# Kernel optimization log

Measured on AMD Instinct MI355X. Metric: run time of the kernel, lower is better.

Reference implementation:

```python
import jax, jax.numpy as jnp
import numpy as np

H = 16        # query heads
KVH = 4       # kv heads
DK = 64       # head dim
D = H * DK    # d_model = 1024
R = 16        # lora rank
SCALING = 16.0 / 16.0 * 1.0   # alpha/rank*scale
ALIBI_ALPHA = 1.0
NEG = jnp.finfo(jnp.float32).min


def _lora_linear(x, W, A, Bm):
    # nn.Linear(bias=False) + LoRA: x@W + (x@A@B)*scaling
    return x @ W + (x @ A @ Bm) * SCALING


def setup_inputs() -> dict:
    key = jax.random.key(0)
    ks = jax.random.split(key, 16)
    B, S = 2, 2048
    f = jnp.float32
    return {
        "query": jax.random.normal(ks[0], (B, S, D), f),
        "key": jax.random.normal(ks[1], (B, S, D), f),
        "value": jax.random.normal(ks[2], (B, S, D), f),
        "Wq": jax.random.normal(ks[3], (D, D), f) * 0.02,
        "Wk": jax.random.normal(ks[4], (D, KVH * DK), f) * 0.02,
        "Wv": jax.random.normal(ks[5], (D, KVH * DK), f) * 0.02,
        "Wo": jax.random.normal(ks[6], (D, D), f) * 0.02,
        "Aq": jax.random.normal(ks[7], (D, R), f) * 0.02,
        "Bq": jax.random.normal(ks[8], (R, D), f) * 0.02,
        "Ak": jax.random.normal(ks[9], (D, R), f) * 0.02,
        "Bk": jax.random.normal(ks[10], (R, KVH * DK), f) * 0.02,
        "Av": jax.random.normal(ks[11], (D, R), f) * 0.02,
        "Bv": jax.random.normal(ks[12], (R, KVH * DK), f) * 0.02,
        "Ao": jax.random.normal(ks[13], (D, R), f) * 0.02,
        "Bo": jax.random.normal(ks[14], (R, D), f) * 0.02,
    }


def _attention(query, key, value, Wq, Wk, Wv, Wo, Aq, Bq, Ak, Bk, Av, Bv, Ao, Bo):
    B, Sq, _ = query.shape
    Sk = key.shape[1]
    groups = H // KVH

    Q = _lora_linear(query, Wq, Aq, Bq).reshape(B, Sq, H, DK).transpose(0, 2, 1, 3)     # (B,H,Sq,DK)
    K = _lora_linear(key, Wk, Ak, Bk).reshape(B, Sk, KVH, DK).transpose(0, 2, 1, 3)      # (B,KVH,Sk,DK)
    V = _lora_linear(value, Wv, Av, Bv).reshape(B, Sk, KVH, DK).transpose(0, 2, 1, 3)

    # GQA: repeat_interleave kv heads to match query heads
    K = jnp.repeat(K, groups, axis=1)   # (B,H,Sk,DK)
    V = jnp.repeat(V, groups, axis=1)

    scale = 1.0 / np.sqrt(DK).astype(np.float32)
    scores = (jnp.einsum('bhqd,bhkd->bhqk', Q, K) * scale).astype(jnp.float32)

    # ALiBi: bias[h,q,k] = slope_h * (k - q), slopes = 2^(-alpha*(i+start)), i=1..H
    slopes = (2.0 ** (-ALIBI_ALPHA * jnp.arange(1, H + 1, dtype=jnp.float32)))
    q_idx = jnp.arange(Sq, dtype=jnp.float32)[:, None]
    k_idx = jnp.arange(Sk, dtype=jnp.float32)[None, :]
    scores = scores + slopes[None, :, None, None] * (k_idx - q_idx)[None, None, :, :]

    # causal mask (keep lower triangle)
    causal = jnp.tril(jnp.ones((Sq, Sk), dtype=bool))
    scores = jnp.where(causal[None, None], scores, NEG)

    attn = jax.nn.softmax(scores, axis=-1).astype(Q.dtype)   # dropout is identity in eval
    x = jnp.einsum('bhqk,bhkd->bhqd', attn, V)
    x = x.transpose(0, 2, 1, 3).reshape(B, Sq, D)
    return _lora_linear(x, Wo, Ao, Bo)


def reference(query, key, value, Wq, Wk, Wv, Wo, Aq, Bq, Ak, Bk, Av, Bv, Ao, Bo):
    return _attention(query, key, value, Wq, Wk, Wv, Wo, Aq, Bq, Ak, Bk, Av, Bv, Ao, Bo)
```

## Files before the change

kernel.cpp:

```cpp
#include <hip/hip_runtime.h>
#include <hip/hip_bf16.h>


typedef __attribute__((ext_vector_type(8))) short short8;
typedef __attribute__((ext_vector_type(4))) float f32x4;
typedef __attribute__((ext_vector_type(16))) float f32x16;
typedef __attribute__((ext_vector_type(2))) unsigned int uint2v;
typedef __attribute__((ext_vector_type(4))) unsigned short ushort4v;

#define DEV static __device__ __forceinline__

DEV unsigned short f32_to_bf16(float f) {
  unsigned int u = __float_as_uint(f);
  u += 0x7FFFu + ((u >> 16) & 1u);
  return (unsigned short)(u >> 16);
}

DEV unsigned int cvt_pk_bf16(float lo, float hi) {
  unsigned int r;
  asm("v_cvt_pk_bf16_f32 %0, %1, %2" : "=v"(r) : "v"(lo), "v"(hi));
  return r;
}

DEV float fexp2(float x) { return __builtin_amdgcn_exp2f(x); }

DEV short8 cvt8(f32x4 a, f32x4 b) {
  short8 r;
  r[0] = (short)f32_to_bf16(a[0]); r[1] = (short)f32_to_bf16(a[1]);
  r[2] = (short)f32_to_bf16(a[2]); r[3] = (short)f32_to_bf16(a[3]);
  r[4] = (short)f32_to_bf16(b[0]); r[5] = (short)f32_to_bf16(b[1]);
  r[6] = (short)f32_to_bf16(b[2]); r[7] = (short)f32_to_bf16(b[3]);
  return r;
}

DEV void gld16(const unsigned short* g, unsigned short* l) {
  __builtin_amdgcn_global_load_lds(
      (const __attribute__((address_space(1))) void*)g,
      (__attribute__((address_space(3))) void*)l,
      16, 0, 0);
}

DEV int xcd_chunk(int bid, int nblk) {
  const int chunk = nblk >> 3;
  return (bid & 7) * chunk + (bid >> 3);
}

__global__ __launch_bounds__(256) void weff_all_kernel(
    const float* __restrict__ Wq, const float* __restrict__ Aq, const float* __restrict__ Bq, unsigned short* __restrict__ WqT,
    const float* __restrict__ Wk, const float* __restrict__ Ak, const float* __restrict__ Bk, unsigned short* __restrict__ WkT,
    const float* __restrict__ Wv, const float* __restrict__ Av, const float* __restrict__ Bv, unsigned short* __restrict__ WvT,
    const float* __restrict__ Wo, const float* __restrict__ Ao, const float* __restrict__ Bo, unsigned short* __restrict__ WoT) {
  __shared__ float tile[16][17];
  const int bx = blockIdx.x;
  const float *W, *A, *Bm; unsigned short* WT; int N, nb;
  if (bx < 64)       { W = Wq; A = Aq; Bm = Bq; WT = WqT; N = 1024; nb = bx; }
  else if (bx < 80)  { W = Wk; A = Ak; Bm = Bk; WT = WkT; N = 256;  nb = bx - 64; }
  else if (bx < 96)  { W = Wv; A = Av; Bm = Bv; WT = WvT; N = 256;  nb = bx - 80; }
  else               { W = Wo; A = Ao; Bm = Bo; WT = WoT; N = 1024; nb = bx - 96; }
  const int tx = threadIdx.x, ty = threadIdx.y;
  const int n0 = nb * 16, k0 = blockIdx.y * 16;
  const int n = n0 + tx, k = k0 + ty;
  float acc = W[(size_t)k * N + n];
#pragma unroll
  for (int r = 0; r < 16; ++r) acc += A[k * 16 + r] * Bm[(size_t)r * N + n];
  tile[ty][tx] = acc;
  __syncthreads();
  WT[(size_t)(n0 + ty) * 1024 + (k0 + tx)] = f32_to_bf16(tile[tx][ty]);
}

__global__ __launch_bounds__(256) void cast3_kernel(const float* __restrict__ q,
                                                    const float* __restrict__ k,
                                                    const float* __restrict__ v,
                                                    unsigned short* __restrict__ oq,
                                                    unsigned short* __restrict__ ok,
                                                    unsigned short* __restrict__ ov) {
  const int seg = blockIdx.x >> 11;
  const size_t off = ((size_t)(blockIdx.x & 2047) * 256 + threadIdx.x) * 8;
  const float* src = (seg == 0) ? q : (seg == 1) ? k : v;
  unsigned short* dst = (seg == 0) ? oq : (seg == 1) ? ok : ov;
  f32x4 a = *(const f32x4*)(src + off);
  f32x4 b = *(const f32x4*)(src + off + 4);
  *(short8*)(dst + off) = cvt8(a, b);
}

template <int OUTMODE>
DEV void gemm97_core(const unsigned short* __restrict__ X,
                     const unsigned short* __restrict__ WT,
                     void* __restrict__ Cv, int N, int m0b, int n0b,
                     unsigned short* lds) {
  constexpr int K = 1024, BK = 64, NT = K / BK;
  constexpr int ASZ = 64 * 64;
  constexpr int BUFE = ASZ + 128 * 64;
  const int tid = threadIdx.x;
  const int w = tid >> 6, l = tid & 63;
  const int lr = l & 15, lg = l >> 4;
  const int wm = w >> 1, wn = w & 1;
  const int srow = l >> 3, schunk = l & 7;

  const unsigned short* Xrow0 = X + (size_t)m0b * K;
  const unsigned short* Wrow0 = WT + (size_t)n0b * K;

  f32x4 acc[2][4];
#pragma unroll
  for (int mm = 0; mm < 2; ++mm)
#pragma unroll
    for (int nn = 0; nn < 4; ++nn) acc[mm][nn] = f32x4{0.f, 0.f, 0.f, 0.f};

#define STAGE(T, BUF)                                                        \
  {                                                                          \
    unsigned short* Ab_ = lds + (BUF) * BUFE;                                \
    unsigned short* Bb_ = Ab_ + ASZ;                                         \
    const int k0_ = (T) * BK;                                                \
    _Pragma("unroll")                                                        \
    for (int ii = 0; ii < 2; ++ii) {                                         \
      const int inst_ = 2 * w + ii;                                          \
      const int row_ = inst_ * 8 + srow;                                     \
      const int cs_ = (schunk ^ (row_ & 7)) * 8;                             \
      gld16(Xrow0 + (size_t)row_ * K + k0_ + cs_, Ab_ + inst_ * 512);        \
    }                                                                        \
    _Pragma("unroll")                                                        \
    for (int ii = 0; ii < 4; ++ii) {                                         \
      const int inst_ = 4 * w + ii;                                          \
      const int row_ = inst_ * 8 + srow;                                     \
      const int cs_ = (schunk ^ (row_ & 7)) * 8;                             \
      gld16(Wrow0 + (size_t)row_ * K + k0_ + cs_, Bb_ + inst_ * 512);        \
    }                                                                        \
  }

  STAGE(0, 0)
  __syncthreads();
  int cur = 0;

  for (int t = 0; t < NT; ++t) {
    if (t + 1 < NT) STAGE(t + 1, cur ^ 1)

    const unsigned short* Ab = lds + cur * BUFE;
    const unsigned short* Bb = Ab + ASZ;
    short8 af[2][2], bfg[4][2];
#pragma unroll
    for (int kk = 0; kk < 2; ++kk) {
#pragma unroll
      for (int mm = 0; mm < 2; ++mm) {
        const int row = wm * 32 + mm * 16 + lr;
        const int cc = ((kk * 4 + lg) ^ (row & 7)) * 8;
        af[mm][kk] = *(const short8*)(Ab + row * 64 + cc);
      }
#pragma unroll
      for (int nn = 0; nn < 4; ++nn) {
        const int row = wn * 64 + nn * 16 + lr;
        const int cc = ((kk * 4 + lg) ^ (row & 7)) * 8;
        bfg[nn][kk] = *(const short8*)(Bb + row * 64 + cc);
      }
    }

#pragma unroll
    for (int kk = 0; kk < 2; ++kk)
#pragma unroll
      for (int mm = 0; mm < 2; ++mm)
#pragma unroll
        for (int nn = 0; nn < 4; ++nn)
          acc[mm][nn] = __builtin_amdgcn_mfma_f32_16x16x32_bf16(af[mm][kk], bfg[nn][kk], acc[mm][nn], 0, 0, 0);

    __syncthreads();
    cur ^= 1;
  }
#undef STAGE

#pragma unroll
  for (int mm = 0; mm < 2; ++mm)
#pragma unroll
    for (int nn = 0; nn < 4; ++nn)
#pragma unroll
      for (int i = 0; i < 4; ++i) {
        const int row = m0b + wm * 32 + mm * 16 + lg * 4 + i;
        const int col = n0b + wn * 64 + nn * 16 + lr;
        const float v = acc[mm][nn][i];
        if (OUTMODE == 0) {
          ((unsigned short*)Cv)[(size_t)row * N + col] = f32_to_bf16(v);
        } else if (OUTMODE == 1) {
          ((float*)Cv)[(size_t)row * N + col] = v;
        } else if (OUTMODE == 2) {
          ((unsigned short*)Cv)[((size_t)((row >> 11) * 4 + (col >> 6)) * 64 + (col & 63)) * 2048 + (row & 2047)] = f32_to_bf16(v);
        } else {
          ((unsigned short*)Cv)[((size_t)((row >> 11) * 4 + (col >> 6)) * 2048 + (row & 2047)) * 64 + (col & 63)] = f32_to_bf16(v);
        }
      }
}

__global__ __launch_bounds__(256, 3) void qkv_kernel(
    const unsigned short* __restrict__ Xq, const unsigned short* __restrict__ Xk, const unsigned short* __restrict__ Xv,
    const unsigned short* __restrict__ WqT, const unsigned short* __restrict__ WkT, const unsigned short* __restrict__ WvT,
    unsigned short* __restrict__ Qw, unsigned short* __restrict__ Khm, unsigned short* __restrict__ Vtw) {
  __shared__ __align__(16) unsigned short lds[2 * (64 * 64 + 128 * 64)];
  const int bx = blockIdx.x;
  if (bx < 512) {
    const int v = xcd_chunk(bx, 512);
    gemm97_core<0>(Xq, WqT, Qw, 1024, (v >> 3) * 64, (v & 7) * 128, lds);
  } else if (bx < 640) {
    const int v = xcd_chunk(bx - 512, 128);
    gemm97_core<3>(Xk, WkT, Khm, 256, (v >> 1) * 64, (v & 1) * 128, lds);
  } else {
    const int v = xcd_chunk(bx - 640, 128);
    gemm97_core<2>(Xv, WvT, Vtw, 256, (v >> 1) * 64, (v & 1) * 128, lds);
  }
}

__global__ __launch_bounds__(256, 3) void ogemm_kernel(const unsigned short* __restrict__ Xw,
                                                       const unsigned short* __restrict__ WoT,
                                                       float* __restrict__ out) {
  __shared__ __align__(16) unsigned short lds[2 * (64 * 64 + 128 * 64)];
  const int v = xcd_chunk(blockIdx.x, 512);
  gemm97_core<1>(Xw, WoT, out, 1024, (v >> 3) * 64, (v & 7) * 128, lds);
}

__global__ __launch_bounds__(512, 4) void attn8_kernel(const unsigned short* __restrict__ Q,
                                                       const unsigned short* __restrict__ Kh,
                                                       const unsigned short* __restrict__ Vt,
                                                       unsigned short* __restrict__ Xo) {
  __shared__ __align__(16) unsigned short sbuf[2][2][2][4096];

  const int tid = threadIdx.x;
  const int l = tid & 63, w = tid >> 6;
  const int cq = l & 31, hi = l >> 5;
  const int qc = w & 3, par = w >> 2;

  const int bid = blockIdx.x;
  const int half = bid >> 8, p = bid & 255;
  const int h = p & 15, b = (p >> 4) & 1, j = p >> 5;
  const int qt = half ? j : 15 - j;

  const int kv = h >> 2;
  const int qw0 = qt * 128 + qc * 32;
  const int q = qw0 + cq;
  const float LOG2E = 1.44269504f;
  const float slope2 = fexp2(-(float)(h + 1)) * LOG2E;
  const float qscale = 0.125f * LOG2E;

  const unsigned short* qp = Q + ((size_t)(b * 2048 + q)) * 1024 + h * 64 + hi * 8;
  short8 qf[4];
#pragma unroll
  for (int c = 0; c < 4; ++c) qf[c] = *(const short8*)(qp + c * 16);

  const int nit = qt + 1;
  const int nktw = (qw0 + 31) / 64 + 1;

  const unsigned short* Kg = Kh + (size_t)(b * 4 + kv) * 2048 * 64;
  const unsigned short* Vg = Vt + (size_t)(b * 4 + kv) * 64 * 2048;
  const int srow = tid >> 3;
  const int scol = (tid & 7) ^ (srow & 7);
  const unsigned short* ksrc = Kg + srow * 64 + scol * 8;
  const unsigned short* vsrc = Vg + (size_t)srow * 2048 + scol * 8;
  const size_t woff = (size_t)w * 512;

#define STAGE(IT, B_)                                                       \
  {                                                                         \
    const int kb_ = (IT) * 128;                                             \
    gld16(ksrc + (size_t)kb_ * 64,        &sbuf[B_][0][0][woff]);           \
    gld16(ksrc + (size_t)(kb_ + 64) * 64, &sbuf[B_][0][1][woff]);           \
    gld16(vsrc + kb_,                     &sbuf[B_][1][0][woff]);           \
    gld16(vsrc + kb_ + 64,                &sbuf[B_][1][1][woff]);           \
  }

  STAGE(0, 0)
  __syncthreads();
  int cur = 0;

  f32x16 oA, oB;
#pragma unroll
  for (int r = 0; r < 16; ++r) { oA[r] = 0.f; oB[r] = 0.f; }
  float mrun = -3e38f, lrun = 0.f;

  const float fhi = 4.0f * (float)hi;
  const int sx = cq & 7;
  const int rA = cq, rB = cq + 32;

  for (int it = 0; it < nit; ++it) {
    if (it + 1 < nit) STAGE(it + 1, cur ^ 1)

    const int kt = 2 * it + par;
    if (kt < nktw) {
      const int k0 = kt * 64;
      const unsigned short* Kl = &sbuf[cur][0][par][0];
      const unsigned short* Vl = &sbuf[cur][1][par][0];

      f32x16 sA, sB;
#pragma unroll
      for (int r = 0; r < 16; ++r) { sA[r] = 0.f; sB[r] = 0.f; }
      __builtin_amdgcn_s_setprio(1);
#pragma unroll
      for (int c = 0; c < 4; ++c) {
        short8 ka = *(const short8*)(Kl + rA * 64 + (((c * 2 + hi) ^ sx) * 8));
        short8 kb = *(const short8*)(Kl + rB * 64 + (((c * 2 + hi) ^ sx) * 8));
        sA = __builtin_amdgcn_mfma_f32_32x32x16_bf16(ka, qf[c], sA, 0, 0, 0);
        sB = __builtin_amdgcn_mfma_f32_32x32x16_bf16(kb, qf[c], sB, 0, 0, 0);
      }
      __builtin_amdgcn_s_setprio(0);

      const float fhb   = fmaf(slope2, fhi, slope2 * (float)(k0 - q));
      const float fhb32 = fmaf(slope2, fhi, slope2 * (float)(k0 + 32 - q));
      const bool masked = (kt == nktw - 1);
      const int ikq4 = k0 - q + 4 * hi;
      float svA[16], svB[16];
#pragma unroll
      for (int r = 0; r < 16; ++r) {
        const int koffc = (r & 3) + 8 * (r >> 2);
        const float kf = (float)koffc;
        float va = fmaf(sA[r], qscale, fmaf(slope2, kf, fhb));
        float vb = fmaf(sB[r], qscale, fmaf(slope2, kf, fhb32));
        if (masked) {
          if (ikq4 + koffc > 0) va = -3e38f;
          if (ikq4 + koffc + 32 > 0) vb = -3e38f;
        }
        svA[r] = va; svB[r] = vb;
      }

      float m0_ = fmaxf(svA[0], svB[0]), m1_ = fmaxf(svA[1], svB[1]);
      float m2_ = fmaxf(svA[2], svB[2]), m3_ = fmaxf(svA[3], svB[3]);
#pragma unroll
      for (int r = 4; r < 16; r += 4) {
        m0_ = fmaxf(m0_, fmaxf(svA[r], svB[r]));
        m1_ = fmaxf(m1_, fmaxf(svA[r + 1], svB[r + 1]));
        m2_ = fmaxf(m2_, fmaxf(svA[r + 2], svB[r + 2]));
        m3_ = fmaxf(m3_, fmaxf(svA[r + 3], svB[r + 3]));
      }
      float mx = fmaxf(fmaxf(m0_, m1_), fmaxf(m2_, m3_));
      mx = fmaxf(mx, __shfl_xor(mx, 32));

      if (!__all(mx <= mrun + 8.0f)) {
        const float mnew = fmaxf(mrun, mx);
        const float fsc = fexp2(mrun - mnew);
        lrun *= fsc;
        mrun = mnew;
#pragma unroll
        for (int r = 0; r < 16; ++r) { oA[r] *= fsc; oB[r] *= fsc; }
      }

      float pA[16], pB[16];
      float l0_ = 0.f, l1_ = 0.f, l2_ = 0.f, l3_ = 0.f;
#pragma unroll
      for (int r = 0; r < 16; r += 4) {
        pA[r] = fexp2(svA[r] - mrun);         pB[r] = fexp2(svB[r] - mrun);
        pA[r + 1] = fexp2(svA[r + 1] - mrun); pB[r + 1] = fexp2(svB[r + 1] - mrun);
        pA[r + 2] = fexp2(svA[r + 2] - mrun); pB[r + 2] = fexp2(svB[r + 2] - mrun);
        pA[r + 3] = fexp2(svA[r + 3] - mrun); pB[r + 3] = fexp2(svB[r + 3] - mrun);
        l0_ += pA[r] + pB[r];
        l1_ += pA[r + 1] + pB[r + 1];
        l2_ += pA[r + 2] + pB[r + 2];
        l3_ += pA[r + 3] + pB[r + 3];
      }
      float ls = (l0_ + l1_) + (l2_ + l3_);
      ls += __shfl_xor(ls, 32);
      lrun += ls;

#define PV_HALF(PARR, KHALF)                                                          \
      {                                                                               \
        _Pragma("unroll")                                                             \
        for (int g = 0; g < 2; ++g) {                                                 \
          unsigned int a0 = cvt_pk_bf16(PARR[g * 8 + 0], PARR[g * 8 + 1]);            \
          unsigned int b0 = cvt_pk_bf16(PARR[g * 8 + 4], PARR[g * 8 + 5]);            \
          unsigned int a1 = cvt_pk_bf16(PARR[g * 8 + 2], PARR[g * 8 + 3]);            \
          unsigned int b1 = cvt_pk_bf16(PARR[g * 8 + 6], PARR[g * 8 + 7]);            \
          uint2v r0 = __builtin_amdgcn_permlane32_swap(a0, b0, false, false);         \
          uint2v r1 = __builtin_amdgcn_permlane32_swap(a1, b1, false, false);         \
          union { unsigned int u[4]; short8 s; } pb_;                                 \
          pb_.u[0] = r0[0]; pb_.u[1] = r1[0]; pb_.u[2] = r0[1]; pb_.u[3] = r1[1];     \
          const int c16 = ((KHALF) * 4 + g * 2 + hi) ^ sx;                            \
          short8 v0 = *(const short8*)(Vl + rA * 64 + c16 * 8);                       \
          short8 v1 = *(const short8*)(Vl + rB * 64 + c16 * 8);                       \
          __builtin_amdgcn_s_setprio(1);                                              \
          oA = __builtin_amdgcn_mfma_f32_32x32x16_bf16(v0, pb_.s, oA, 0, 0, 0);       \
          oB = __builtin_amdgcn_mfma_f32_32x32x16_bf16(v1, pb_.s, oB, 0, 0, 0);       \
          __builtin_amdgcn_s_setprio(0);                                              \
        }                                                                             \
      }
      PV_HALF(pA, 0)
      PV_HALF(pB, 1)
#undef PV_HALF
    }

    __syncthreads();
    cur ^= 1;
  }
#undef STAGE

  float* obuf = (float*)&sbuf[0][0][0][0];
  float* mlb  = obuf + 128 * 68;
  const int orow = (qc * 32 + cq) * 68;

  if (par == 1) {
#pragma unroll
    for (int g = 0; g < 4; ++g) {
      f32x4 t0 = {oA[g * 4 + 0], oA[g * 4 + 1], oA[g * 4 + 2], oA[g * 4 + 3]};
      f32x4 t1 = {oB[g * 4 + 0], oB[g * 4 + 1], oB[g * 4 + 2], oB[g * 4 + 3]};
      *(f32x4*)&obuf[orow + g * 8 + 4 * hi] = t0;
      *(f32x4*)&obuf[orow + 32 + g * 8 + 4 * hi] = t1;
    }
    if (hi == 0) {
      mlb[(qc * 32 + cq) * 2] = mrun;
      mlb[(qc * 32 + cq) * 2 + 1] = lrun;
    }
  }
  __syncthreads();
  if (par == 0) {
    const float m1v = mlb[(qc * 32 + cq) * 2];
    const float l1v = mlb[(qc * 32 + cq) * 2 + 1];
    const float ms = fmaxf(mrun, m1v);
    const float s0 = fexp2(mrun - ms), s1 = fexp2(m1v - ms);
    const float rinv = __builtin_amdgcn_rcpf(fmaf(lrun, s0, l1v * s1));
    unsigned short* op = Xo + ((size_t)(b * 2048 + q)) * 1024 + h * 64;
#pragma unroll
    for (int g = 0; g < 4; ++g) {
      const int d0 = g * 8 + 4 * hi;
      f32x4 u0 = *(const f32x4*)&obuf[orow + d0];
      f32x4 u1 = *(const f32x4*)&obuf[orow + 32 + d0];
      ushort4v t0, t1;
#pragma unroll
      for (int i = 0; i < 4; ++i) {
        t0[i] = f32_to_bf16(fmaf(oA[g * 4 + i], s0, u0[i] * s1) * rinv);
        t1[i] = f32_to_bf16(fmaf(oB[g * 4 + i], s0, u1[i] * s1) * rinv);
      }
      *(ushort4v*)(op + d0) = t0;
      *(ushort4v*)(op + 32 + d0) = t1;
    }
  }
}

extern "C" void kernel_launch(void* const* d_in, const int* in_sizes, int n_in,
                              void* d_out, int out_size, void* d_ws, size_t ws_size,
                              hipStream_t stream) {
  const float* query = (const float*)d_in[0];
  const float* key   = (const float*)d_in[1];
  const float* value = (const float*)d_in[2];
  const float* Wq = (const float*)d_in[3];
  const float* Wk = (const float*)d_in[4];
  const float* Wv = (const float*)d_in[5];
  const float* Wo = (const float*)d_in[6];
  const float* Aq = (const float*)d_in[7];
  const float* Bq = (const float*)d_in[8];
  const float* Ak = (const float*)d_in[9];
  const float* Bk = (const float*)d_in[10];
  const float* Av = (const float*)d_in[11];
  const float* Bv = (const float*)d_in[12];
  const float* Ao = (const float*)d_in[13];
  const float* Bo = (const float*)d_in[14];

  unsigned short* ws  = (unsigned short*)d_ws;
  unsigned short* WqT = ws;
  unsigned short* WkT = WqT + 1024 * 1024;
  unsigned short* WvT = WkT + 256 * 1024;
  unsigned short* WoT = WvT + 256 * 1024;
  unsigned short* Qw  = WoT + 1024 * 1024;
  unsigned short* Khm = Qw + 4096 * 1024;
  unsigned short* Vtw = Khm + 4096 * 256;
  unsigned short* Xw  = Vtw + 4096 * 256;
  unsigned short* Xcq = Xw + 4096 * 1024;
  unsigned short* Xck = Xcq + 4096 * 1024;

  weff_all_kernel<<<dim3(160, 64), dim3(16, 16), 0, stream>>>(
      Wq, Aq, Bq, WqT, Wk, Ak, Bk, WkT, Wv, Av, Bv, WvT, Wo, Ao, Bo, WoT);

  cast3_kernel<<<6144, 256, 0, stream>>>(query, key, value, Xcq, Xck, Xw);

  qkv_kernel<<<768, 256, 0, stream>>>(Xcq, Xck, Xw, WqT, WkT, WvT, Qw, Khm, Vtw);

  attn8_kernel<<<512, 512, 0, stream>>>(Qw, Khm, Vtw, Xw);

  ogemm_kernel<<<512, 256, 0, stream>>>(Xw, WoT, (float*)d_out);
}
```

Baseline: 101.2 us.

## Split attention KV across four waves per block and fuse prep kernels

The attention kernel now gives each block 64 query rows instead of 128, and the key dimension is split four ways across wave pairs, with a 4-way softmax merge through LDS at the end. The grid doubles to 1024 blocks, scheduled longest-first. K/V tiles are loaded 256 keys at a time into a single buffer, with no double-buffered prefetch. Separately, the weight-merge and input-cast kernels are fused into one launch to remove a kernel launch. The risk is that dropping the prefetch exposes load latency, and the merge costs more LDS traffic.

```diff
diff --git a/kernel.cpp b/kernel.cpp
--- a/kernel.cpp
+++ b/kernel.cpp
@@ -45,42 +45,41 @@
   return (bid & 7) * chunk + (bid >> 3);
 }
 
-__global__ __launch_bounds__(256) void weff_all_kernel(
+__global__ __launch_bounds__(256) void prep_kernel(
     const float* __restrict__ Wq, const float* __restrict__ Aq, const float* __restrict__ Bq, unsigned short* __restrict__ WqT,
     const float* __restrict__ Wk, const float* __restrict__ Ak, const float* __restrict__ Bk, unsigned short* __restrict__ WkT,
     const float* __restrict__ Wv, const float* __restrict__ Av, const float* __restrict__ Bv, unsigned short* __restrict__ WvT,
-    const float* __restrict__ Wo, const float* __restrict__ Ao, const float* __restrict__ Bo, unsigned short* __restrict__ WoT) {
+    const float* __restrict__ Wo, const float* __restrict__ Ao, const float* __restrict__ Bo, unsigned short* __restrict__ WoT,
+    const float* __restrict__ q, const float* __restrict__ k, const float* __restrict__ v,
+    unsigned short* __restrict__ oq, unsigned short* __restrict__ ok, unsigned short* __restrict__ ov) {
+  const int bx = blockIdx.x;
+  if (bx < 6144) {
+    const int seg = bx >> 11;
+    const size_t off = ((size_t)(bx & 2047) * 256 + threadIdx.x) * 8;
+    const float* src = (seg == 0) ? q : (seg == 1) ? k : v;
+    unsigned short* dst = (seg == 0) ? oq : (seg == 1) ? ok : ov;
+    f32x4 a = *(const f32x4*)(src + off);
+    f32x4 b = *(const f32x4*)(src + off + 4);
+    *(short8*)(dst + off) = cvt8(a, b);
+    return;
+  }
   __shared__ float tile[16][17];
-  const int bx = blockIdx.x;
+  const int wb = bx - 6144;
+  const int nbx = wb % 160, kby = wb / 160;
   const float *W, *A, *Bm; unsigned short* WT; int N, nb;
-  if (bx < 64)       { W = Wq; A = Aq; Bm = Bq; WT = WqT; N = 1024; nb = bx; }
-  else if (bx < 80)  { W = Wk; A = Ak; Bm = Bk; WT = WkT; N = 256;  nb = bx - 64; }
-  else if (bx < 96)  { W = Wv; A = Av; Bm = Bv; WT = WvT; N = 256;  nb = bx - 80; }
-  else               { W = Wo; A = Ao; Bm = Bo; WT = WoT; N = 1024; nb = bx - 96; }
-  const int tx = threadIdx.x, ty = threadIdx.y;
-  const int n0 = nb * 16, k0 = blockIdx.y * 16;
-  const int n = n0 + tx, k = k0 + ty;
-  float acc = W[(size_t)k * N + n];
-#pragma unroll
-  for (int r = 0; r < 16; ++r) acc += A[k * 16 + r] * Bm[(size_t)r * N + n];
+  if (nbx < 64)       { W = Wq; A = Aq; Bm = Bq; WT = WqT; N = 1024; nb = nbx; }
+  else if (nbx < 80)  { W = Wk; A = Ak; Bm = Bk; WT = WkT; N = 256;  nb = nbx - 64; }
+  else if (nbx < 96)  { W = Wv; A = Av; Bm = Bv; WT = WvT; N = 256;  nb = nbx - 80; }
+  else                { W = Wo; A = Ao; Bm = Bo; WT = WoT; N = 1024; nb = nbx - 96; }
+  const int tx = threadIdx.x & 15, ty = threadIdx.x >> 4;
+  const int n0 = nb * 16, k0 = kby * 16;
+  const int n = n0 + tx, kk = k0 + ty;
+  float acc = W[(size_t)kk * N + n];
+#pragma unroll
+  for (int r = 0; r < 16; ++r) acc += A[kk * 16 + r] * Bm[(size_t)r * N + n];
   tile[ty][tx] = acc;
   __syncthreads();
   WT[(size_t)(n0 + ty) * 1024 + (k0 + tx)] = f32_to_bf16(tile[tx][ty]);
-}
-
-__global__ __launch_bounds__(256) void cast3_kernel(const float* __restrict__ q,
-                                                    const float* __restrict__ k,
-                                                    const float* __restrict__ v,
-                                                    unsigned short* __restrict__ oq,
-                                                    unsigned short* __restrict__ ok,
-                                                    unsigned short* __restrict__ ov) {
-  const int seg = blockIdx.x >> 11;
-  const size_t off = ((size_t)(blockIdx.x & 2047) * 256 + threadIdx.x) * 8;
-  const float* src = (seg == 0) ? q : (seg == 1) ? k : v;
-  unsigned short* dst = (seg == 0) ? oq : (seg == 1) ? ok : ov;
-  f32x4 a = *(const f32x4*)(src + off);
-  f32x4 b = *(const f32x4*)(src + off + 4);
-  *(short8*)(dst + off) = cvt8(a, b);
 }
 
 template <int OUTMODE>
@@ -213,24 +212,25 @@
   gemm97_core<1>(Xw, WoT, out, 1024, (v >> 3) * 64, (v & 7) * 128, lds);
 }
 
-__global__ __launch_bounds__(512, 4) void attn8_kernel(const unsigned short* __restrict__ Q,
+__global__ __launch_bounds__(512, 4) void attn9_kernel(const unsigned short* __restrict__ Q,
                                                        const unsigned short* __restrict__ Kh,
                                                        const unsigned short* __restrict__ Vt,
                                                        unsigned short* __restrict__ Xo) {
-  __shared__ __align__(16) unsigned short sbuf[2][2][2][4096];
+  __shared__ __align__(16) unsigned short sbuf[2][4][4096];
 
   const int tid = threadIdx.x;
   const int l = tid & 63, w = tid >> 6;
   const int cq = l & 31, hi = l >> 5;
-  const int qc = w & 3, par = w >> 2;
+  const int cq2 = w & 1, ks = w >> 1;
 
   const int bid = blockIdx.x;
-  const int half = bid >> 8, p = bid & 255;
-  const int h = p & 15, b = (p >> 4) & 1, j = p >> 5;
-  const int qt = half ? j : 15 - j;
+  const int s = 31 - (bid >> 5);
+  const int rem = bid & 31;
+  const int h = rem & 15, b = rem >> 4;
 
   const int kv = h >> 2;
-  const int qw0 = qt * 128 + qc * 32;
+  const int c_abs = 2 * s + cq2;
+  const int qw0 = c_abs * 32;
   const int q = qw0 + cq;
   const float LOG2E = 1.44269504f;
   const float slope2 = fexp2(-(float)(h + 1)) * LOG2E;
@@ -241,8 +241,8 @@
 #pragma unroll
   for (int c = 0; c < 4; ++c) qf[c] = *(const short8*)(qp + c * 16);
 
-  const int nit = qt + 1;
-  const int nktw = (qw0 + 31) / 64 + 1;
+  const int T = (c_abs >> 1) + 1;
+  const int NI = (s + 4) >> 2;
 
   const unsigned short* Kg = Kh + (size_t)(b * 4 + kv) * 2048 * 64;
   const unsigned short* Vg = Vt + (size_t)(b * 4 + kv) * 64 * 2048;
@@ -252,19 +252,6 @@
   const unsigned short* vsrc = Vg + (size_t)srow * 2048 + scol * 8;
   const size_t woff = (size_t)w * 512;
 
-#define STAGE(IT, B_)                                                       \
-  {                                                                         \
-    const int kb_ = (IT) * 128;                                             \
-    gld16(ksrc + (size_t)kb_ * 64,        &sbuf[B_][0][0][woff]);           \
-    gld16(ksrc + (size_t)(kb_ + 64) * 64, &sbuf[B_][0][1][woff]);           \
-    gld16(vsrc + kb_,                     &sbuf[B_][1][0][woff]);           \
-    gld16(vsrc + kb_ + 64,                &sbuf[B_][1][1][woff]);           \
-  }
-
-  STAGE(0, 0)
-  __syncthreads();
-  int cur = 0;
-
   f32x16 oA, oB;
 #pragma unroll
   for (int r = 0; r < 16; ++r) { oA[r] = 0.f; oB[r] = 0.f; }
@@ -274,14 +261,20 @@
   const int sx = cq & 7;
   const int rA = cq, rB = cq + 32;
 
-  for (int it = 0; it < nit; ++it) {
-    if (it + 1 < nit) STAGE(it + 1, cur ^ 1)
-
-    const int kt = 2 * it + par;
-    if (kt < nktw) {
+  for (int it = 0; it < NI; ++it) {
+    const int kb = it * 256;
+#pragma unroll
+    for (int t = 0; t < 4; ++t) {
+      gld16(ksrc + (size_t)(kb + 64 * t) * 64, &sbuf[0][t][woff]);
+      gld16(vsrc + (kb + 64 * t), &sbuf[1][t][woff]);
+    }
+    __syncthreads();
+
+    const int kt = 4 * it + ks;
+    if (kt < T) {
       const int k0 = kt * 64;
-      const unsigned short* Kl = &sbuf[cur][0][par][0];
-      const unsigned short* Vl = &sbuf[cur][1][par][0];
+      const unsigned short* Kl = &sbuf[0][kt & 3][0];
+      const unsigned short* Vl = &sbuf[1][kt & 3][0];
 
       f32x16 sA, sB;
 #pragma unroll
@@ -290,15 +283,15 @@
 #pragma unroll
       for (int c = 0; c < 4; ++c) {
         short8 ka = *(const short8*)(Kl + rA * 64 + (((c * 2 + hi) ^ sx) * 8));
-        short8 kb = *(const short8*)(Kl + rB * 64 + (((c * 2 + hi) ^ sx) * 8));
+        short8 kb2 = *(const short8*)(Kl + rB * 64 + (((c * 2 + hi) ^ sx) * 8));
         sA = __builtin_amdgcn_mfma_f32_32x32x16_bf16(ka, qf[c], sA, 0, 0, 0);
-        sB = __builtin_amdgcn_mfma_f32_32x32x16_bf16(kb, qf[c], sB, 0, 0, 0);
+        sB = __builtin_amdgcn_mfma_f32_32x32x16_bf16(kb2, qf[c], sB, 0, 0, 0);
       }
       __builtin_amdgcn_s_setprio(0);
 
       const float fhb   = fmaf(slope2, fhi, slope2 * (float)(k0 - q));
       const float fhb32 = fmaf(slope2, fhi, slope2 * (float)(k0 + 32 - q));
-      const bool masked = (kt == nktw - 1);
+      const bool masked = (kt == T - 1);
       const int ikq4 = k0 - q + 4 * hi;
       float svA[16], svB[16];
 #pragma unroll
@@ -379,45 +372,63 @@
     }
 
     __syncthreads();
-    cur ^= 1;
-  }
-#undef STAGE
-
-  float* obuf = (float*)&sbuf[0][0][0][0];
-  float* mlb  = obuf + 128 * 68;
-  const int orow = (qc * 32 + cq) * 68;
-
-  if (par == 1) {
+  }
+
+  float* obuf = (float*)&sbuf[0][0][0];
+  float* mlb  = obuf + 3 * 64 * 68;
+  const int prow = cq2 * 32 + cq;
+
+  if (ks > 0) {
+    const int row = (ks - 1) * 64 + prow;
 #pragma unroll
     for (int g = 0; g < 4; ++g) {
       f32x4 t0 = {oA[g * 4 + 0], oA[g * 4 + 1], oA[g * 4 + 2], oA[g * 4 + 3]};
       f32x4 t1 = {oB[g * 4 + 0], oB[g * 4 + 1], oB[g * 4 + 2], oB[g * 4 + 3]};
-      *(f32x4*)&obuf[orow + g * 8 + 4 * hi] = t0;
-      *(f32x4*)&obuf[orow + 32 + g * 8 + 4 * hi] = t1;
-    }
-    if (hi == 0) {
-      mlb[(qc * 32 + cq) * 2] = mrun;
-      mlb[(qc * 32 + cq) * 2 + 1] = lrun;
-    }
+      *(f32x4*)&obuf[row * 68 + g * 8 + 4 * hi] = t0;
+      *(f32x4*)&obuf[row * 68 + 32 + g * 8 + 4 * hi] = t1;
+    }
+    if (hi == 0) { mlb[row * 2] = mrun; mlb[row * 2 + 1] = lrun; }
   }
   __syncthreads();
-  if (par == 0) {
-    const float m1v = mlb[(qc * 32 + cq) * 2];
-    const float l1v = mlb[(qc * 32 + cq) * 2 + 1];
-    const float ms = fmaxf(mrun, m1v);
-    const float s0 = fexp2(mrun - ms), s1 = fexp2(m1v - ms);
-    const float rinv = __builtin_amdgcn_rcpf(fmaf(lrun, s0, l1v * s1));
+  if (ks == 0) {
+    float mp[3], lp[3];
+#pragma unroll
+    for (int p = 0; p < 3; ++p) {
+      mp[p] = mlb[(p * 64 + prow) * 2];
+      lp[p] = mlb[(p * 64 + prow) * 2 + 1];
+    }
+    const float ms = fmaxf(fmaxf(mrun, mp[0]), fmaxf(mp[1], mp[2]));
+    const float s0 = fexp2(mrun - ms);
+    float sp[3];
+    float lst = lrun * s0;
+#pragma unroll
+    for (int p = 0; p < 3; ++p) {
+      sp[p] = fexp2(mp[p] - ms);
+      lst = fmaf(lp[p], sp[p], lst);
+    }
+    const float rinv = __builtin_amdgcn_rcpf(lst);
     unsigned short* op = Xo + ((size_t)(b * 2048 + q)) * 1024 + h * 64;
 #pragma unroll
     for (int g = 0; g < 4; ++g) {
       const int d0 = g * 8 + 4 * hi;
-      f32x4 u0 = *(const f32x4*)&obuf[orow + d0];
-      f32x4 u1 = *(const f32x4*)&obuf[orow + 32 + d0];
+      float a0[4], a1[4];
+#pragma unroll
+      for (int i = 0; i < 4; ++i) { a0[i] = oA[g * 4 + i] * s0; a1[i] = oB[g * 4 + i] * s0; }
+#pragma unroll
+      for (int p = 0; p < 3; ++p) {
+        f32x4 u0 = *(const f32x4*)&obuf[(p * 64 + prow) * 68 + d0];
+        f32x4 u1 = *(const f32x4*)&obuf[(p * 64 + prow) * 68 + 32 + d0];
+#pragma unroll
+        for (int i = 0; i < 4; ++i) {
+          a0[i] = fmaf(u0[i], sp[p], a0[i]);
+          a1[i] = fmaf(u1[i], sp[p], a1[i]);
+        }
+      }
       ushort4v t0, t1;
 #pragma unroll
       for (int i = 0; i < 4; ++i) {
-        t0[i] = f32_to_bf16(fmaf(oA[g * 4 + i], s0, u0[i] * s1) * rinv);
-        t1[i] = f32_to_bf16(fmaf(oB[g * 4 + i], s0, u1[i] * s1) * rinv);
+        t0[i] = f32_to_bf16(a0[i] * rinv);
+        t1[i] = f32_to_bf16(a1[i] * rinv);
       }
       *(ushort4v*)(op + d0) = t0;
       *(ushort4v*)(op + 32 + d0) = t1;
@@ -456,14 +467,13 @@
   unsigned short* Xcq = Xw + 4096 * 1024;
   unsigned short* Xck = Xcq + 4096 * 1024;
 
-  weff_all_kernel<<<dim3(160, 64), dim3(16, 16), 0, stream>>>(
-      Wq, Aq, Bq, WqT, Wk, Ak, Bk, WkT, Wv, Av, Bv, WvT, Wo, Ao, Bo, WoT);
-
-  cast3_kernel<<<6144, 256, 0, stream>>>(query, key, value, Xcq, Xck, Xw);
+  prep_kernel<<<16384, 256, 0, stream>>>(
+      Wq, Aq, Bq, WqT, Wk, Ak, Bk, WkT, Wv, Av, Bv, WvT, Wo, Ao, Bo, WoT,
+      query, key, value, Xcq, Xck, Xw);
 
   qkv_kernel<<<768, 256, 0, stream>>>(Xcq, Xck, Xw, WqT, WkT, WvT, Qw, Khm, Vtw);
 
-  attn8_kernel<<<512, 512, 0, stream>>>(Qw, Khm, Vtw, Xw);
+  attn9_kernel<<<1024, 512, 0, stream>>>(Qw, Khm, Vtw, Xw);
 
   ogemm_kernel<<<512, 256, 0, stream>>>(Xw, WoT, (float*)d_out);
 }
```

Measured after the change: 103.3 us. +2.1%, slower.
